# Kernel tuning notes

Hardware: AMD Instinct MI355X
Metric: run time of the kernel (lower is better)

The kernel has to match this reference:

```python
import jax, jax.numpy as jnp
import numpy as np

B, T, FEAT, MD, PROJ, DEC = 32768, 50, 14, 3, 128, 128
DT = 0.1           # hard-coded integration step in original rollout
ALPHA = 0.3        # keras LeakyReLU default alpha
DUMMY_DX = 50.0    # dummy_value_set['em_delta_x']
DUMMY_DV = 0.0     # dummy_value_set['em_delta_v']


def setup_inputs() -> dict:
    key = jax.random.key(0)
    ks = jax.random.split(key, 12)
    d_in = PROJ + DEC + 8 + MD  # 267
    idm_s = jax.random.normal(ks[2], (B, T, FEAT), jnp.float32)
    # last feature is the m_veh_exists 0/1 flag
    idm_s = idm_s.at[:, :, -1].set((idm_s[:, :, -1] > 0).astype(jnp.float32))
    return {
        "proj_latent": jax.random.normal(ks[0], (B, PROJ), jnp.float32),
        "enc_h": jax.random.normal(ks[1], (B, DEC), jnp.float32),
        "idm_s": idm_s,
        "merger_cs": jax.random.normal(ks[3], (B, T, MD), jnp.float32),
        "env_mean": jax.random.normal(ks[4], (8,), jnp.float32),
        "env_var": jax.random.uniform(ks[5], (8,), jnp.float32) + 0.5,  # keep away from 0
        "W1": jax.random.normal(ks[6], (d_in, DEC), jnp.float32) * 0.05,
        "b1": jnp.zeros((DEC,), jnp.float32),
        "W2": jax.random.normal(ks[7], (DEC, DEC), jnp.float32) * 0.05,
        "b2": jnp.zeros((DEC,), jnp.float32),
        "W3": jax.random.normal(ks[8], (DEC, 1), jnp.float32) * 0.05,
        "b3": jnp.zeros((1,), jnp.float32),
    }


def _leaky(x):
    return jnp.where(x >= 0, x, ALPHA * x)


def reference(proj_latent, enc_h, idm_s, merger_cs, env_mean, env_var,
              W1, b1, W2, b2, W3, b3):
    inv_std = 1.0 / jnp.sqrt(env_var)  # scale_env_s uses var_**0.5

    def mlp(x):  # att_layer_1 -> att_layer_2 -> action_neu
        h = _leaky(x @ W1 + b1)
        h = _leaky(h @ W2 + b2)
        return h @ W3 + b3  # [B,1]

    # initial physics state from timestep 0
    ego_v0 = idm_s[:, 0, 0:1]    # [B,1]
    ego_a0 = idm_s[:, 0, 11:12]
    ego_x0 = idm_s[:, 0, 3:4]
    disp0 = jnp.zeros_like(ego_v0)

    def step(carry, xs):
        ego_v, ego_a, ego_x, disp = carry
        idm_t, mc_t = xs  # [B,FEAT], [B,MD]  (timestep step-1)
        f_veh_v = idm_t[:, 1:2]
        m_veh_v = idm_t[:, 2:3]
        f_glob_x = idm_t[:, 4:5]
        m_glob_x = idm_t[:, 5:6]
        f_veh_a = idm_t[:, 12:13]
        m_exists = idm_t[:, -1:]
        ef_dx = f_glob_x - ego_x
        em_dx = (m_glob_x - ego_x) * m_exists + (1.0 - m_exists) * DUMMY_DX
        ef_dv = ego_v - f_veh_v
        em_dv = (ego_v - m_veh_v) * m_exists + (1.0 - m_exists) * DUMMY_DV
        env = jnp.concatenate([ego_v, f_veh_v, ego_a, f_veh_a,
                               ef_dv, ef_dx, em_dv, em_dx], axis=-1)  # [B,8]
        env = (env - env_mean) * inv_std
        inp = jnp.concatenate([proj_latent, enc_h, env, mc_t], axis=-1)  # [B,267]
        a_new = mlp(inp)  # [B,1]
        move = ego_v * DT + 0.5 * a_new * DT * DT
        disp_new = disp + move
        ego_x_new = ego_x + move
        ego_v_new = ego_v + a_new * DT
        return (ego_v_new, a_new, ego_x_new, disp_new), (a_new, disp_new)

    xs = (jnp.swapaxes(idm_s, 0, 1), jnp.swapaxes(merger_cs, 0, 1))  # [T,B,*]
    _, (acts, disps) = jax.lax.scan(step, (ego_v0, ego_a0, ego_x0, disp0), xs)
    act_seq = jnp.swapaxes(acts, 0, 1)    # [B,T,1]
    disp_seq = jnp.swapaxes(disps, 0, 1)  # [B,T,1]
    displacement_seq = jnp.concatenate([disp0[:, None, :], disp_seq], axis=1)  # [B,T+1,1]
    return displacement_seq, act_seq
```

## Files before the change

kernel.cpp:

```cpp
#include <hip/hip_runtime.h>


using bf16x8 = __attribute__((ext_vector_type(8))) short;
using f32x16 = __attribute__((ext_vector_type(16))) float;
using u32x4  = __attribute__((ext_vector_type(4))) unsigned int;

constexpr int B_TOT   = 32768;
constexpr int T_STEPS = 50;
constexpr int FEATC   = 14;
constexpr int MDC     = 3;
constexpr float ALPHA_C = 0.3f;
constexpr float DT_C    = 0.1f;

constexpr int NB   = 32;
constexpr int NTHR = 256;
constexpr int PS   = 132;
constexpr int ENVS = 18;

__device__ __forceinline__ float leaky(float x) { return fmaxf(x, ALPHA_C * x); }

__device__ __forceinline__ short2 split1(float x) {
    unsigned u = __float_as_uint(x);
    short h = (short)(u >> 16);
    float r = x - __uint_as_float(u & 0xFFFF0000u);
    short l = (short)(__float_as_uint(r) >> 16);
    return make_short2(h, l);
}

__device__ __forceinline__ unsigned packsplit(float x) {
    unsigned u = __float_as_uint(x);
    float r = x - __uint_as_float(u & 0xFFFF0000u);
    return (u >> 16) | (__float_as_uint(r) & 0xFFFF0000u);
}

#define MFMA(A, B, C) __builtin_amdgcn_mfma_f32_32x32x16_bf16(A, B, C, 0, 0, 0)

__launch_bounds__(NTHR, 2)
__global__ void fwd_sim(const float* __restrict__ proj,
                        const float* __restrict__ enc,
                        const float* __restrict__ idm,
                        const float* __restrict__ mc,
                        const float* __restrict__ env_mean,
                        const float* __restrict__ env_var,
                        const float* __restrict__ W1,
                        const float* __restrict__ b1,
                        const float* __restrict__ W2,
                        const float* __restrict__ b2,
                        const float* __restrict__ W3,
                        const float* __restrict__ b3,
                        float* __restrict__ out)
{
    __shared__ unsigned s_h1p[NB * PS];
    __shared__ float    s_p  [NB * PS];
    __shared__ float    s_env[NB * ENVS];

    const int tid  = threadIdx.x;
    const int lane = tid & 63;
    const int nq   = (tid >> 6) & 3;
    const int l31  = lane & 31;
    const int half = lane >> 5;
    const int ncol = nq * 32 + l31;
    const int am   = l31;
    const int b_base = blockIdx.x * NB;
    const long ACT_OFF = (long)B_TOT * 51;

    for (int i = tid; i < NB * ENVS; i += NTHR) s_env[i] = 0.f;
    __syncthreads();

    const float b1v = b1[ncol];
    const float b2v = b2[ncol];
    const float w3v = W3[ncol];

    unsigned*       wp = s_h1p + (4 * half) * PS + ncol;
    const unsigned* rp = s_h1p + am * PS + half * 8;
    float*          pw = s_p   + (4 * half) * PS + ncol;

    bf16x8 w2h[8], w2l[8];
    for (int kb = 0; kb < 8; ++kb) {
        #pragma unroll
        for (int j = 0; j < 8; ++j) {
            short2 s = split1(W2[(kb * 16 + half * 8 + j) * 128 + ncol]);
            w2h[kb][j] = s.x; w2l[kb][j] = s.y;
        }
    }
    bf16x8 w1xh, w1xl;
    #pragma unroll
    for (int j = 0; j < 8; ++j) {
        int k = half * 8 + j;
        short2 s = split1(k < 11 ? W1[(256 + k) * 128 + ncol] : 0.f);
        w1xh[j] = s.x; w1xl[j] = s.y;
    }

    f32x16 base;
    #pragma unroll
    for (int r = 0; r < 16; ++r) base[r] = b1v;
    for (int kb = 0; kb < 16; ++kb) {
        const float* src = (kb < 8) ? proj : enc;
        const int kloc = (kb & 7) * 16 + half * 8;
        const float* ap = src + (long)(b_base + am) * 128 + kloc;
        float av[8];
        *(float4*)(av)     = *(const float4*)(ap);
        *(float4*)(av + 4) = *(const float4*)(ap + 4);
        bf16x8 ah, al, bh, bl;
        #pragma unroll
        for (int j = 0; j < 8; ++j) {
            short2 s = split1(av[j]);
            ah[j] = s.x; al[j] = s.y;
        }
        #pragma unroll
        for (int j = 0; j < 8; ++j) {
            short2 s = split1(W1[(kb * 16 + half * 8 + j) * 128 + ncol]);
            bh[j] = s.x; bl[j] = s.y;
        }
        base = MFMA(ah, bh, base);
        base = MFMA(al, bh, base);
        base = MFMA(ah, bl, base);
    }

    const bool act = (tid & 7) == 0;
    const int  sm  = tid >> 3;
    const long sb  = b_base + sm;
    float ego_v = 0.f, ego_a = 0.f, ego_x = 0.f, disp = 0.f, b3r = 0.f;
    float mn[8], is[8];
    float nv1 = 0.f, nv2 = 0.f, nv4 = 0.f, nv5 = 0.f, nv12 = 0.f, nv13 = 0.f;
    float nm0 = 0.f, nm1 = 0.f, nm2 = 0.f;
    if (act) {
        #pragma unroll
        for (int k = 0; k < 8; ++k) { mn[k] = env_mean[k]; is[k] = rsqrtf(env_var[k]); }
        b3r = b3[0];
        const float* r0 = idm + sb * (T_STEPS * FEATC);
        const float* m0 = mc  + sb * (T_STEPS * MDC);
        ego_v = r0[0]; ego_a = r0[11]; ego_x = r0[3]; disp = 0.f;
        out[sb * 51] = 0.f;
        float e[8];
        e[0] = ego_v; e[1] = r0[1]; e[2] = ego_a; e[3] = r0[12];
        e[4] = ego_v - r0[1];
        e[5] = r0[4] - ego_x;
        e[6] = (ego_v - r0[2]) * r0[13];
        e[7] = (r0[5] - ego_x) * r0[13] + (1.f - r0[13]) * 50.f;
        #pragma unroll
        for (int k = 0; k < 8; ++k) s_env[sm * ENVS + k] = (e[k] - mn[k]) * is[k];
        s_env[sm * ENVS + 8]  = m0[0];
        s_env[sm * ENVS + 9]  = m0[1];
        s_env[sm * ENVS + 10] = m0[2];
        nv1 = r0[FEATC + 1]; nv2 = r0[FEATC + 2]; nv4 = r0[FEATC + 4];
        nv5 = r0[FEATC + 5]; nv12 = r0[FEATC + 12]; nv13 = r0[FEATC + 13];
        nm0 = m0[MDC]; nm1 = m0[MDC + 1]; nm2 = m0[MDC + 2];
    }
    __syncthreads();

    for (int t = 0; t < T_STEPS; ++t) {
        {
            const float* ep = s_env + am * ENVS + half * 8;
            float av[8];
            *(float2*)(av)     = *(const float2*)(ep);
            *(float2*)(av + 2) = *(const float2*)(ep + 2);
            *(float2*)(av + 4) = *(const float2*)(ep + 4);
            *(float2*)(av + 6) = *(const float2*)(ep + 6);
            bf16x8 ah, al;
            #pragma unroll
            for (int j = 0; j < 8; ++j) {
                short2 s = split1(av[j]);
                ah[j] = s.x; al[j] = s.y;
            }
            f32x16 acc = base;
            acc = MFMA(ah, w1xh, acc);
            acc = MFMA(al, w1xh, acc);
            acc = MFMA(ah, w1xl, acc);
            #pragma unroll
            for (int r = 0; r < 16; ++r) {
                const int roff = (r & 3) + 8 * (r >> 2);
                wp[roff * PS] = packsplit(leaky(acc[r]));
            }
        }
        __syncthreads();

        {
            f32x16 acc;
            #pragma unroll
            for (int r = 0; r < 16; ++r) acc[r] = b2v;
            #pragma unroll
            for (int kb = 0; kb < 8; ++kb) {
                u32x4 q0 = *reinterpret_cast<const u32x4*>(rp + kb * 16);
                u32x4 q1 = *reinterpret_cast<const u32x4*>(rp + kb * 16 + 4);
                u32x4 hh, ll;
                hh[0] = __builtin_amdgcn_perm(q0[1], q0[0], 0x05040100u);
                hh[1] = __builtin_amdgcn_perm(q0[3], q0[2], 0x05040100u);
                hh[2] = __builtin_amdgcn_perm(q1[1], q1[0], 0x05040100u);
                hh[3] = __builtin_amdgcn_perm(q1[3], q1[2], 0x05040100u);
                ll[0] = __builtin_amdgcn_perm(q0[1], q0[0], 0x07060302u);
                ll[1] = __builtin_amdgcn_perm(q0[3], q0[2], 0x07060302u);
                ll[2] = __builtin_amdgcn_perm(q1[1], q1[0], 0x07060302u);
                ll[3] = __builtin_amdgcn_perm(q1[3], q1[2], 0x07060302u);
                bf16x8 ah2 = __builtin_bit_cast(bf16x8, hh);
                bf16x8 al2 = __builtin_bit_cast(bf16x8, ll);
                acc = MFMA(ah2, w2h[kb], acc);
                acc = MFMA(al2, w2h[kb], acc);
                acc = MFMA(ah2, w2l[kb], acc);
            }
            #pragma unroll
            for (int r = 0; r < 16; ++r) {
                const int roff = (r & 3) + 8 * (r >> 2);
                pw[roff * PS] = leaky(acc[r]) * w3v;
            }
        }
        __syncthreads();

        {
            const int row = tid >> 3, seg = tid & 7;
            const float* pp = s_p + row * PS + seg * 16;
            float s = 0.f;
            #pragma unroll
            for (int i = 0; i < 8; ++i) {
                float2 v = *(const float2*)(pp + i * 2);
                s += v.x + v.y;
            }
            s += __shfl_xor(s, 1);
            s += __shfl_xor(s, 2);
            s += __shfl_xor(s, 4);
            if (act) {
                const float a = s + b3r;
                const float move = ego_v * DT_C + 0.5f * a * DT_C * DT_C;
                disp  += move;
                ego_x += move;
                ego_v += a * DT_C;
                ego_a  = a;
                out[sb * 51 + t + 1] = disp;
                out[ACT_OFF + sb * 50 + t] = a;
                if (t < T_STEPS - 1) {
                    float e[8];
                    e[0] = ego_v; e[1] = nv1; e[2] = ego_a; e[3] = nv12;
                    e[4] = ego_v - nv1;
                    e[5] = nv4 - ego_x;
                    e[6] = (ego_v - nv2) * nv13;
                    e[7] = (nv5 - ego_x) * nv13 + (1.f - nv13) * 50.f;
                    #pragma unroll
                    for (int k = 0; k < 8; ++k) s_env[sm * ENVS + k] = (e[k] - mn[k]) * is[k];
                    s_env[sm * ENVS + 8]  = nm0;
                    s_env[sm * ENVS + 9]  = nm1;
                    s_env[sm * ENVS + 10] = nm2;
                    const int tn = (t + 2 < T_STEPS) ? t + 2 : T_STEPS - 1;
                    const float* rn = idm + sb * (T_STEPS * FEATC) + tn * FEATC;
                    const float* mrn = mc + sb * (T_STEPS * MDC) + tn * MDC;
                    nv1 = rn[1]; nv2 = rn[2]; nv4 = rn[4]; nv5 = rn[5];
                    nv12 = rn[12]; nv13 = rn[13];
                    nm0 = mrn[0]; nm1 = mrn[1]; nm2 = mrn[2];
                }
            }
        }
        __syncthreads();
    }
}

extern "C" void kernel_launch(void* const* d_in, const int* in_sizes, int n_in,
                              void* d_out, int out_size, void* d_ws, size_t ws_size,
                              hipStream_t stream) {
    const float* proj     = (const float*)d_in[0];
    const float* enc      = (const float*)d_in[1];
    const float* idm      = (const float*)d_in[2];
    const float* mcs      = (const float*)d_in[3];
    const float* env_mean = (const float*)d_in[4];
    const float* env_var  = (const float*)d_in[5];
    const float* W1       = (const float*)d_in[6];
    const float* b1       = (const float*)d_in[7];
    const float* W2       = (const float*)d_in[8];
    const float* b2       = (const float*)d_in[9];
    const float* W3       = (const float*)d_in[10];
    const float* b3       = (const float*)d_in[11];

    fwd_sim<<<B_TOT / NB, NTHR, 0, stream>>>(
        proj, enc, idm, mcs, env_mean, env_var,
        W1, b1, W2, b2, W3, b3, (float*)d_out);
}
```

Before: 387.1 us.

## Keep env state in registers per lane and fuse layer-3 reduction into MFMA epilogue

Every lane now redundantly holds the physics state for its row and builds the env MFMA operand in registers, which removes the shared-memory env buffer and one barrier per timestep. The second MFMA swaps its operands so each lane owns output columns for a row. Bias, leaky and W3 dot are then applied in registers, and partial sums are reduced through a small shared array instead of a full 32x128 staging buffer. This cuts LDS traffic and synchronisation on the serial time loop, at the cost of redundant scalar work and global loads in every wave.

```diff
diff --git a/kernel.cpp b/kernel.cpp
--- a/kernel.cpp
+++ b/kernel.cpp
@@ -15,7 +15,6 @@
 constexpr int NB   = 32;
 constexpr int NTHR = 256;
 constexpr int PS   = 132;
-constexpr int ENVS = 18;
 
 __device__ __forceinline__ float leaky(float x) { return fmaxf(x, ALPHA_C * x); }
 
@@ -51,29 +50,26 @@
                         float* __restrict__ out)
 {
     __shared__ unsigned s_h1p[NB * PS];
-    __shared__ float    s_p  [NB * PS];
-    __shared__ float    s_env[NB * ENVS];
+    __shared__ float    s_part[NB * 4];
+    __shared__ float    s_bw[256];
 
     const int tid  = threadIdx.x;
     const int lane = tid & 63;
-    const int nq   = (tid >> 6) & 3;
+    const int nq   = tid >> 6;
     const int l31  = lane & 31;
     const int half = lane >> 5;
     const int ncol = nq * 32 + l31;
-    const int am   = l31;
     const int b_base = blockIdx.x * NB;
     const long ACT_OFF = (long)B_TOT * 51;
 
-    for (int i = tid; i < NB * ENVS; i += NTHR) s_env[i] = 0.f;
-    __syncthreads();
-
-    const float b1v = b1[ncol];
-    const float b2v = b2[ncol];
-    const float w3v = W3[ncol];
-
-    unsigned*       wp = s_h1p + (4 * half) * PS + ncol;
-    const unsigned* rp = s_h1p + am * PS + half * 8;
-    float*          pw = s_p   + (4 * half) * PS + ncol;
+    for (int i = tid; i < 128; i += NTHR) {
+        s_bw[2 * i]     = b2[i];
+        s_bw[2 * i + 1] = W3[i];
+    }
+
+    unsigned*       wp  = s_h1p + (4 * half) * PS + ncol;
+    const unsigned* rp  = s_h1p + l31 * PS + half * 8;
+    const float*    bwp = s_bw + 2 * (nq * 32 + 4 * half);
 
     bf16x8 w2h[8], w2l[8];
     for (int kb = 0; kb < 8; ++kb) {
@@ -91,13 +87,14 @@
         w1xh[j] = s.x; w1xl[j] = s.y;
     }
 
+    const float b1v = b1[ncol];
     f32x16 base;
     #pragma unroll
     for (int r = 0; r < 16; ++r) base[r] = b1v;
     for (int kb = 0; kb < 16; ++kb) {
         const float* src = (kb < 8) ? proj : enc;
         const int kloc = (kb & 7) * 16 + half * 8;
-        const float* ap = src + (long)(b_base + am) * 128 + kloc;
+        const float* ap = src + (long)(b_base + l31) * 128 + kloc;
         float av[8];
         *(float4*)(av)     = *(const float4*)(ap);
         *(float4*)(av + 4) = *(const float4*)(ap + 4);
@@ -117,56 +114,53 @@
         base = MFMA(ah, bl, base);
     }
 
-    const bool act = (tid & 7) == 0;
-    const int  sm  = tid >> 3;
-    const long sb  = b_base + sm;
-    float ego_v = 0.f, ego_a = 0.f, ego_x = 0.f, disp = 0.f, b3r = 0.f;
+    const long sbr = b_base + l31;
+    const float* idp = idm + sbr * (long)(T_STEPS * FEATC);
+    const float* mcp = mc  + sbr * (long)(T_STEPS * MDC);
     float mn[8], is[8];
+    #pragma unroll
+    for (int k = 0; k < 8; ++k) { mn[k] = env_mean[k]; is[k] = rsqrtf(env_var[k]); }
+    const float b3r = b3[0];
+
+    float ego_v = 0.f, ego_x = 0.f, disp = 0.f;
     float nv1 = 0.f, nv2 = 0.f, nv4 = 0.f, nv5 = 0.f, nv12 = 0.f, nv13 = 0.f;
     float nm0 = 0.f, nm1 = 0.f, nm2 = 0.f;
-    if (act) {
-        #pragma unroll
-        for (int k = 0; k < 8; ++k) { mn[k] = env_mean[k]; is[k] = rsqrtf(env_var[k]); }
-        b3r = b3[0];
-        const float* r0 = idm + sb * (T_STEPS * FEATC);
-        const float* m0 = mc  + sb * (T_STEPS * MDC);
-        ego_v = r0[0]; ego_a = r0[11]; ego_x = r0[3]; disp = 0.f;
-        out[sb * 51] = 0.f;
-        float e[8];
-        e[0] = ego_v; e[1] = r0[1]; e[2] = ego_a; e[3] = r0[12];
-        e[4] = ego_v - r0[1];
-        e[5] = r0[4] - ego_x;
-        e[6] = (ego_v - r0[2]) * r0[13];
-        e[7] = (r0[5] - ego_x) * r0[13] + (1.f - r0[13]) * 50.f;
-        #pragma unroll
-        for (int k = 0; k < 8; ++k) s_env[sm * ENVS + k] = (e[k] - mn[k]) * is[k];
-        s_env[sm * ENVS + 8]  = m0[0];
-        s_env[sm * ENVS + 9]  = m0[1];
-        s_env[sm * ENVS + 10] = m0[2];
-        nv1 = r0[FEATC + 1]; nv2 = r0[FEATC + 2]; nv4 = r0[FEATC + 4];
-        nv5 = r0[FEATC + 5]; nv12 = r0[FEATC + 12]; nv13 = r0[FEATC + 13];
-        nm0 = m0[MDC]; nm1 = m0[MDC + 1]; nm2 = m0[MDC + 2];
-    }
-    __syncthreads();
+    bf16x8 ahe, ale;
+    {
+        float v8[8];
+        if (half == 0) {
+            ego_v = idp[0]; ego_x = idp[3]; disp = 0.f;
+            const float a0 = idp[11];
+            v8[0] = (ego_v - mn[0]) * is[0];
+            v8[1] = (idp[1] - mn[1]) * is[1];
+            v8[2] = (a0 - mn[2]) * is[2];
+            v8[3] = (idp[12] - mn[3]) * is[3];
+            v8[4] = (ego_v - idp[1] - mn[4]) * is[4];
+            v8[5] = (idp[4] - ego_x - mn[5]) * is[5];
+            v8[6] = ((ego_v - idp[2]) * idp[13] - mn[6]) * is[6];
+            v8[7] = ((idp[5] - ego_x) * idp[13] + (1.f - idp[13]) * 50.f - mn[7]) * is[7];
+            nv1 = idp[FEATC + 1];  nv2 = idp[FEATC + 2];
+            nv4 = idp[FEATC + 4];  nv5 = idp[FEATC + 5];
+            nv12 = idp[FEATC + 12]; nv13 = idp[FEATC + 13];
+        } else {
+            v8[0] = mcp[0]; v8[1] = mcp[1]; v8[2] = mcp[2];
+            v8[3] = 0.f; v8[4] = 0.f; v8[5] = 0.f; v8[6] = 0.f; v8[7] = 0.f;
+            nm0 = mcp[MDC]; nm1 = mcp[MDC + 1]; nm2 = mcp[MDC + 2];
+        }
+        #pragma unroll
+        for (int j = 0; j < 8; ++j) {
+            short2 s = split1(v8[j]);
+            ahe[j] = s.x; ale[j] = s.y;
+        }
+        if (nq == 0 && half == 0) out[sbr * 51] = 0.f;
+    }
 
     for (int t = 0; t < T_STEPS; ++t) {
         {
-            const float* ep = s_env + am * ENVS + half * 8;
-            float av[8];
-            *(float2*)(av)     = *(const float2*)(ep);
-            *(float2*)(av + 2) = *(const float2*)(ep + 2);
-            *(float2*)(av + 4) = *(const float2*)(ep + 4);
-            *(float2*)(av + 6) = *(const float2*)(ep + 6);
-            bf16x8 ah, al;
-            #pragma unroll
-            for (int j = 0; j < 8; ++j) {
-                short2 s = split1(av[j]);
-                ah[j] = s.x; al[j] = s.y;
-            }
             f32x16 acc = base;
-            acc = MFMA(ah, w1xh, acc);
-            acc = MFMA(al, w1xh, acc);
-            acc = MFMA(ah, w1xl, acc);
+            acc = MFMA(ahe, w1xh, acc);
+            acc = MFMA(ale, w1xh, acc);
+            acc = MFMA(ahe, w1xl, acc);
             #pragma unroll
             for (int r = 0; r < 16; ++r) {
                 const int roff = (r & 3) + 8 * (r >> 2);
@@ -178,7 +172,7 @@
         {
             f32x16 acc;
             #pragma unroll
-            for (int r = 0; r < 16; ++r) acc[r] = b2v;
+            for (int r = 0; r < 16; ++r) acc[r] = 0.f;
             #pragma unroll
             for (int kb = 0; kb < 8; ++kb) {
                 u32x4 q0 = *reinterpret_cast<const u32x4*>(rp + kb * 16);
@@ -194,61 +188,68 @@
                 ll[3] = __builtin_amdgcn_perm(q1[3], q1[2], 0x07060302u);
                 bf16x8 ah2 = __builtin_bit_cast(bf16x8, hh);
                 bf16x8 al2 = __builtin_bit_cast(bf16x8, ll);
-                acc = MFMA(ah2, w2h[kb], acc);
-                acc = MFMA(al2, w2h[kb], acc);
-                acc = MFMA(ah2, w2l[kb], acc);
-            }
-            #pragma unroll
-            for (int r = 0; r < 16; ++r) {
-                const int roff = (r & 3) + 8 * (r >> 2);
-                pw[roff * PS] = leaky(acc[r]) * w3v;
-            }
+                acc = MFMA(w2h[kb], ah2, acc);
+                acc = MFMA(w2h[kb], al2, acc);
+                acc = MFMA(w2l[kb], ah2, acc);
+            }
+            float ps = 0.f;
+            #pragma unroll
+            for (int g = 0; g < 4; ++g) {
+                const float* bwg = bwp + 16 * g;
+                float4 x0 = *(const float4*)(bwg);
+                float4 x1 = *(const float4*)(bwg + 4);
+                ps += leaky(acc[4 * g + 0] + x0.x) * x0.y;
+                ps += leaky(acc[4 * g + 1] + x0.z) * x0.w;
+                ps += leaky(acc[4 * g + 2] + x1.x) * x1.y;
+                ps += leaky(acc[4 * g + 3] + x1.z) * x1.w;
+            }
+            ps += __shfl_xor(ps, 32);
+            if (half == 0) s_part[l31 * 4 + nq] = ps;
         }
         __syncthreads();
 
         {
-            const int row = tid >> 3, seg = tid & 7;
-            const float* pp = s_p + row * PS + seg * 16;
-            float s = 0.f;
-            #pragma unroll
-            for (int i = 0; i < 8; ++i) {
-                float2 v = *(const float2*)(pp + i * 2);
-                s += v.x + v.y;
-            }
-            s += __shfl_xor(s, 1);
-            s += __shfl_xor(s, 2);
-            s += __shfl_xor(s, 4);
-            if (act) {
-                const float a = s + b3r;
-                const float move = ego_v * DT_C + 0.5f * a * DT_C * DT_C;
-                disp  += move;
-                ego_x += move;
-                ego_v += a * DT_C;
-                ego_a  = a;
-                out[sb * 51 + t + 1] = disp;
-                out[ACT_OFF + sb * 50 + t] = a;
-                if (t < T_STEPS - 1) {
-                    float e[8];
-                    e[0] = ego_v; e[1] = nv1; e[2] = ego_a; e[3] = nv12;
-                    e[4] = ego_v - nv1;
-                    e[5] = nv4 - ego_x;
-                    e[6] = (ego_v - nv2) * nv13;
-                    e[7] = (nv5 - ego_x) * nv13 + (1.f - nv13) * 50.f;
-                    #pragma unroll
-                    for (int k = 0; k < 8; ++k) s_env[sm * ENVS + k] = (e[k] - mn[k]) * is[k];
-                    s_env[sm * ENVS + 8]  = nm0;
-                    s_env[sm * ENVS + 9]  = nm1;
-                    s_env[sm * ENVS + 10] = nm2;
-                    const int tn = (t + 2 < T_STEPS) ? t + 2 : T_STEPS - 1;
-                    const float* rn = idm + sb * (T_STEPS * FEATC) + tn * FEATC;
-                    const float* mrn = mc + sb * (T_STEPS * MDC) + tn * MDC;
+            float4 pp = *(const float4*)(s_part + l31 * 4);
+            const float a = pp.x + pp.y + pp.z + pp.w + b3r;
+            const float move = ego_v * DT_C + 0.5f * a * DT_C * DT_C;
+            disp  += move;
+            ego_x += move;
+            ego_v += a * DT_C;
+            if (nq == 0 && half == 0) {
+                out[sbr * 51 + t + 1] = disp;
+                out[ACT_OFF + sbr * 50 + t] = a;
+            }
+            if (t < T_STEPS - 1) {
+                float v8[8];
+                if (half == 0) {
+                    v8[0] = (ego_v - mn[0]) * is[0];
+                    v8[1] = (nv1 - mn[1]) * is[1];
+                    v8[2] = (a - mn[2]) * is[2];
+                    v8[3] = (nv12 - mn[3]) * is[3];
+                    v8[4] = (ego_v - nv1 - mn[4]) * is[4];
+                    v8[5] = (nv4 - ego_x - mn[5]) * is[5];
+                    v8[6] = ((ego_v - nv2) * nv13 - mn[6]) * is[6];
+                    v8[7] = ((nv5 - ego_x) * nv13 + (1.f - nv13) * 50.f - mn[7]) * is[7];
+                } else {
+                    v8[0] = nm0; v8[1] = nm1; v8[2] = nm2;
+                    v8[3] = 0.f; v8[4] = 0.f; v8[5] = 0.f; v8[6] = 0.f; v8[7] = 0.f;
+                }
+                #pragma unroll
+                for (int j = 0; j < 8; ++j) {
+                    short2 s = split1(v8[j]);
+                    ahe[j] = s.x; ale[j] = s.y;
+                }
+                const int tn = (t + 2 < T_STEPS) ? t + 2 : T_STEPS - 1;
+                if (half == 0) {
+                    const float* rn = idp + tn * FEATC;
                     nv1 = rn[1]; nv2 = rn[2]; nv4 = rn[4]; nv5 = rn[5];
                     nv12 = rn[12]; nv13 = rn[13];
+                } else {
+                    const float* mrn = mcp + tn * MDC;
                     nm0 = mrn[0]; nm1 = mrn[1]; nm2 = mrn[2];
                 }
             }
         }
-        __syncthreads();
     }
 }
 
```

Measured after the change: 404.4 us. +4.5%, slower.
